# Performance work log

Hardware: AMD Instinct MI355X
Metric: run time of the kernel (lower is better)

Reference implementation:

```python
import jax, jax.numpy as jnp
import numpy as np

# Hardcoded hyperparameters from the torch module
E = 128   # n_embd
H = 4     # n_head
HS = 32   # head_size = n_embd // n_head
L = 4     # n_layer
T = 512   # block_size (full context)
V = 512   # vocab_size (quantization_levels)
B = 64    # batch
SCALE = 0.02  # init std per _init_weights


def _ln(x, g, b):
    mu = x.mean(-1, keepdims=True)
    var = ((x - mu) ** 2).mean(-1, keepdims=True)
    return (x - mu) / jnp.sqrt(var + 1e-5) * g + b


def setup_inputs() -> dict:
    key = jax.random.key(0)
    ks = jax.random.split(key, 24)
    rn = lambda k, shape: SCALE * jax.random.normal(k, shape, dtype=jnp.float32)
    return {
        "idx": jax.random.randint(ks[0], (B, T), 0, V),
        "tok_emb": rn(ks[1], (V, E)),
        "pos_emb": rn(ks[2], (T, E)),
        # per-head projections, stacked over layers and heads: x[...,E] @ wq[l,h] -> [...,HS]
        "wq": rn(ks[3], (L, H, E, HS)),
        "wk": rn(ks[4], (L, H, E, HS)),
        "wv": rn(ks[5], (L, H, E, HS)),
        "w_proj": rn(ks[6], (L, E, E)),   # torch Linear weight layout [out, in]
        "b_proj": jnp.zeros((L, E), jnp.float32),
        "ln1_g": jnp.ones((L, E), jnp.float32),
        "ln1_b": jnp.zeros((L, E), jnp.float32),
        "ln2_g": jnp.ones((L, E), jnp.float32),
        "ln2_b": jnp.zeros((L, E), jnp.float32),
        "w1": rn(ks[7], (L, 4 * E, E)),
        "b1": jnp.zeros((L, 4 * E), jnp.float32),
        "w2": rn(ks[8], (L, E, 4 * E)),
        "b2": jnp.zeros((L, E), jnp.float32),
        "lnf_g": jnp.ones((E,), jnp.float32),
        "lnf_b": jnp.zeros((E,), jnp.float32),
        "w_head": rn(ks[9], (V, E)),
        "b_head": jnp.zeros((V,), jnp.float32),
    }


def reference(idx, tok_emb, pos_emb, wq, wk, wv, w_proj, b_proj,
              ln1_g, ln1_b, ln2_g, ln2_b, w1, b1, w2, b2,
              lnf_g, lnf_b, w_head, b_head):
    Bv, Tv = idx.shape
    x = tok_emb[idx] + pos_emb[None, :Tv, :]          # [B,T,E]
    causal = jnp.tril(jnp.ones((Tv, Tv), dtype=bool))
    for l in range(L):
        h = _ln(x, ln1_g[l], ln1_b[l])
        q = jnp.einsum('bte,hed->bhtd', h, wq[l])     # [B,H,T,HS]
        k = jnp.einsum('bte,hed->bhtd', h, wk[l])
        v = jnp.einsum('bte,hed->bhtd', h, wv[l])
        s = jnp.einsum('bhtd,bhsd->bhts', q, k) * (HS ** -0.5)
        s = jnp.where(causal, s, -jnp.inf)
        a = jax.nn.softmax(s, axis=-1)
        o = jnp.einsum('bhts,bhsd->bhtd', a, v)       # [B,H,T,HS]
        o = o.transpose(0, 2, 1, 3).reshape(Bv, Tv, E)  # concat heads
        x = x + o @ w_proj[l].T + b_proj[l]
        h = _ln(x, ln2_g[l], ln2_b[l])
        x = x + jax.nn.gelu(h @ w1[l].T + b1[l], approximate=False) @ w2[l].T + b2[l]
    x = _ln(x, lnf_g, lnf_b)
    logits = x @ w_head.T + b_head                    # [B,T,V]
    return logits
```

## Files before the change

### kernel.cpp

```cpp
#include <hip/hip_runtime.h>

typedef __bf16 bf16x8 __attribute__((ext_vector_type(8)));
typedef __bf16 bf16x2 __attribute__((ext_vector_type(2)));
typedef float f32x4 __attribute__((ext_vector_type(4)));

constexpr int E_ = 128, H_ = 4, HS_ = 32, L_ = 4, T_ = 512, V_ = 512, B_ = 64;
constexpr int M_ = B_ * T_;

__device__ __forceinline__ float b2f(ushort u) {
    return __uint_as_float(((uint)u) << 16);
}
__device__ __forceinline__ ushort f2b(float f) {
    uint x = __float_as_uint(f);
    uint r = (x + 0x7fffu + ((x >> 16) & 1u)) >> 16;
    return (ushort)r;
}
__device__ __forceinline__ uint packbf(float a, float b) {
    bf16x2 t; t[0] = (__bf16)a; t[1] = (__bf16)b;
    return __builtin_bit_cast(uint, t);
}

constexpr int kNSeg = 19;
constexpr int kOffs[kNSeg + 1] = {
    0, 65536, 131072, 196608, 262144, 327680, 393216, 393728, 394240, 394752,
    395264, 395776, 657920, 659968, 922112, 922624, 922752, 922880, 988416, 988928
};
constexpr int kTotal = 988928;

struct SrcPtrs { const void* p[kNSeg]; };

__global__ __launch_bounds__(256) void k_convert(SrcPtrs sp, ushort* __restrict__ arena) {
    int gid = blockIdx.x * 256 + threadIdx.x;
    if (gid >= kTotal) return;
    bool isf32 = (((const uint*)sp.p[7])[0] == 0x3F800000u);
    int s = 0;
    #pragma unroll
    for (int i = 1; i < kNSeg; i++) if (gid >= kOffs[i]) s = i;
    int local = gid - kOffs[s];
    ushort v;
    if (isf32) v = f2b(((const float*)sp.p[s])[local]);
    else       v = ((const ushort*)sp.p[s])[local];
    arena[gid] = v;
}

__global__ void k_prep_qkv(const ushort* __restrict__ wq, const ushort* __restrict__ wk,
                           const ushort* __restrict__ wv, ushort* __restrict__ wt) {
    int gid = blockIdx.x * 256 + threadIdx.x;
    if (gid >= L_ * 384 * E_) return;
    int e = gid & 127;
    int n = (gid >> 7) % 384;
    int l = gid / (384 * E_);
    int part = n >> 7, within = n & 127, hh = within >> 5, d = within & 31;
    const ushort* src = part == 0 ? wq : (part == 1 ? wk : wv);
    wt[gid] = src[(((size_t)(l * H_ + hh) * E_) + e) * HS_ + d];
}

__global__ __launch_bounds__(256) void k_embed_ln(const int* __restrict__ idx,
                                                  const ushort* __restrict__ tok,
                                                  const ushort* __restrict__ pos,
                                                  const ushort* __restrict__ g,
                                                  const ushort* __restrict__ beta,
                                                  float* __restrict__ x, ushort* __restrict__ h) {
    int wave = threadIdx.x >> 6, lane = threadIdx.x & 63;
    int row = blockIdx.x * 4 + wave;
    int t = row & (T_ - 1);
    int id = idx[row];
    float v0 = b2f(tok[id * E_ + lane])      + b2f(pos[t * E_ + lane]);
    float v1 = b2f(tok[id * E_ + lane + 64]) + b2f(pos[t * E_ + lane + 64]);
    size_t o = (size_t)row * E_;
    x[o + lane] = v0; x[o + lane + 64] = v1;
    float s = v0 + v1;
    #pragma unroll
    for (int m = 32; m; m >>= 1) s += __shfl_xor(s, m, 64);
    float mu = s * (1.0f / 128.0f);
    float d0 = v0 - mu, d1 = v1 - mu;
    float ss = d0 * d0 + d1 * d1;
    #pragma unroll
    for (int m = 32; m; m >>= 1) ss += __shfl_xor(ss, m, 64);
    float rstd = rsqrtf(ss * (1.0f / 128.0f) + 1e-5f);
    h[o + lane]      = f2b(d0 * rstd * b2f(g[lane])      + b2f(beta[lane]));
    h[o + lane + 64] = f2b(d1 * rstd * b2f(g[lane + 64]) + b2f(beta[lane + 64]));
}

template<int EPI>
__global__ __launch_bounds__(256) void k_gemm(const ushort* __restrict__ A, const ushort* __restrict__ W,
                                              const ushort* __restrict__ bias, void* __restrict__ outp,
                                              void* __restrict__ outp2,
                                              const ushort* __restrict__ lng, const ushort* __restrict__ lnb,
                                              const uint* __restrict__ dtraw, int K, int lda, int ldc) {
    int wid = threadIdx.x >> 6, lane = threadIdx.x & 63;
    int wr = wid >> 1, wc = wid & 1;
    int bm = blockIdx.x, bn = blockIdx.y;
    int r16 = lane & 15, kq = lane >> 4;
    const ushort* Abase = A + (size_t)(bm * 128 + wr * 64 + r16) * lda + kq * 8;
    const ushort* Wbase = W + (size_t)(bn * 128 + wc * 64 + r16) * K + kq * 8;
    bool f32out = false;
    if constexpr (EPI == 1) f32out = (dtraw[0] == 0x3F800000u);
    f32x4 acc[4][4];
    #pragma unroll
    for (int i = 0; i < 4; i++)
        #pragma unroll
        for (int j = 0; j < 4; j++) acc[i][j] = (f32x4)0.0f;
    for (int k0 = 0; k0 < K; k0 += 32) {
        bf16x8 af[4], wf[4];
        #pragma unroll
        for (int mi = 0; mi < 4; mi++)
            af[mi] = *(const bf16x8*)(Abase + (size_t)mi * 16 * lda + k0);
        #pragma unroll
        for (int ni = 0; ni < 4; ni++)
            wf[ni] = *(const bf16x8*)(Wbase + (size_t)ni * 16 * K + k0);
        #pragma unroll
        for (int mi = 0; mi < 4; mi++)
            #pragma unroll
            for (int ni = 0; ni < 4; ni++)
                acc[mi][ni] = __builtin_amdgcn_mfma_f32_16x16x32_bf16(af[mi], wf[ni], acc[mi][ni], 0, 0, 0);
    }
    int orow0 = bm * 128 + wr * 64 + kq * 4;
    int ocol0 = bn * 128 + wc * 64 + r16;
    if constexpr (EPI == 5) {
        __shared__ float lnS[2][128], lnQ[2][128];
        float*  xg = (float*)outp;
        ushort* hg = (ushort*)outp2;
        #pragma unroll
        for (int ni = 0; ni < 4; ni++) {
            int col = ocol0 + ni * 16;
            float bv = b2f(bias[col]);
            #pragma unroll
            for (int mi = 0; mi < 4; mi++) {
                #pragma unroll
                for (int e = 0; e < 4; e++) {
                    size_t gi = (size_t)(orow0 + mi * 16 + e) * 128 + col;
                    float xv = xg[gi] + acc[mi][ni][e] + bv;
                    xg[gi] = xv;
                    acc[mi][ni][e] = xv;
                }
            }
        }
        #pragma unroll
        for (int mi = 0; mi < 4; mi++) {
            #pragma unroll
            for (int e = 0; e < 4; e++) {
                float s = 0.f, q = 0.f;
                #pragma unroll
                for (int ni = 0; ni < 4; ni++) { float v = acc[mi][ni][e]; s += v; q += v * v; }
                #pragma unroll
                for (int mk = 1; mk < 16; mk <<= 1) {
                    s += __shfl_xor(s, mk, 64); q += __shfl_xor(q, mk, 64);
                }
                if (r16 == 0) {
                    int lrow = wr * 64 + mi * 16 + kq * 4 + e;
                    lnS[wc][lrow] = s; lnQ[wc][lrow] = q;
                }
            }
        }
        __syncthreads();
        float gc[4], bc[4];
        #pragma unroll
        for (int ni = 0; ni < 4; ni++) {
            int col = ocol0 + ni * 16;
            gc[ni] = b2f(lng[col]); bc[ni] = b2f(lnb[col]);
        }
        #pragma unroll
        for (int mi = 0; mi < 4; mi++) {
            #pragma unroll
            for (int e = 0; e < 4; e++) {
                int lrow = wr * 64 + mi * 16 + kq * 4 + e;
                float tot = lnS[0][lrow] + lnS[1][lrow];
                float tq  = lnQ[0][lrow] + lnQ[1][lrow];
                float mu  = tot * (1.0f / 128.0f);
                float var = tq * (1.0f / 128.0f) - mu * mu;
                float rstd = rsqrtf(var + 1e-5f);
                size_t grow = (size_t)(bm * 128 + lrow) * 128;
                #pragma unroll
                for (int ni = 0; ni < 4; ni++) {
                    int col = ocol0 + ni * 16;
                    hg[grow + col] = f2b((acc[mi][ni][e] - mu) * rstd * gc[ni] + bc[ni]);
                }
            }
        }
        return;
    }
    if constexpr (EPI == 4) {
        if (bn == 2) {
            ushort* vt = (ushort*)outp2;
            #pragma unroll
            for (int mi = 0; mi < 4; mi++) {
                int row0 = orow0 + mi * 16;
                int bb = row0 >> 9, tt = row0 & 511;
                #pragma unroll
                for (int ni = 0; ni < 4; ni++) {
                    int vd = (ocol0 - 256) + ni * 16;
                    int hh = vd >> 5, dd = vd & 31;
                    ushort4 pk;
                    pk.x = f2b(acc[mi][ni][0]); pk.y = f2b(acc[mi][ni][1]);
                    pk.z = f2b(acc[mi][ni][2]); pk.w = f2b(acc[mi][ni][3]);
                    *(ushort4*)(vt + (((size_t)(bb * 4 + hh) * 32 + dd) << 9) + tt) = pk;
                }
            }
            return;
        }
    }
    #pragma unroll
    for (int mi = 0; mi < 4; mi++) {
        #pragma unroll
        for (int ni = 0; ni < 4; ni++) {
            int col = ocol0 + ni * 16;
            float bv = 0.0f;
            if constexpr (EPI == 1 || EPI == 2) bv = b2f(bias[col]);
            #pragma unroll
            for (int e = 0; e < 4; e++) {
                int row = orow0 + mi * 16 + e;
                float v = acc[mi][ni][e] + bv;
                if constexpr (EPI == 2) v = 0.5f * v * (1.0f + erff(v * 0.70710678118f));
                if constexpr (EPI == 1) {
                    if (f32out) ((float*)outp)[(size_t)row * ldc + col] = v;
                    else        ((ushort*)outp)[(size_t)row * ldc + col] = f2b(v);
                } else {
                    ((ushort*)outp)[(size_t)row * ldc + col] = f2b(v);
                }
            }
        }
    }
}

constexpr float SC_ = 0.2550348637f;

__device__ __forceinline__ bf16x8 scale8(bf16x8 v, float s) {
    bf16x8 r;
    #pragma unroll
    for (int i = 0; i < 8; i++) r[i] = (__bf16)((float)v[i] * s);
    return r;
}

__device__ __forceinline__ bf16x8 relayoutP(const float* p, int r16, int g) {
    uint pk00 = packbf(p[0], p[1]), pk01 = packbf(p[2], p[3]);
    uint pk10 = packbf(p[4], p[5]), pk11 = packbf(p[6], p[7]);
    int ga = ((g & 1) << 5) + r16;
    int gb = ga + 16;
    uint A0 = (uint)__shfl((int)pk00, ga), A1 = (uint)__shfl((int)pk01, ga);
    uint C0 = (uint)__shfl((int)pk00, gb), C1 = (uint)__shfl((int)pk01, gb);
    uint B0 = (uint)__shfl((int)pk10, ga), B1 = (uint)__shfl((int)pk11, ga);
    uint D0 = (uint)__shfl((int)pk10, gb), D1 = (uint)__shfl((int)pk11, gb);
    bool hi2 = g >= 2;
    uint4 pr;
    pr.x = hi2 ? B0 : A0; pr.y = hi2 ? B1 : A1;
    pr.z = hi2 ? D0 : C0; pr.w = hi2 ? D1 : C1;
    return __builtin_bit_cast(bf16x8, pr);
}

__global__ __launch_bounds__(256) void k_attn_mfma(const ushort* __restrict__ qk,
                                                   const ushort* __restrict__ vt,
                                                   ushort* __restrict__ o) {
    int lane = threadIdx.x & 63, w = threadIdx.x >> 6;
    int id = blockIdx.x;
    int xcd = id & 7, grp = id >> 3;
    int bh = (xcd << 5) | (grp >> 2);
    int qs = grp & 3;
    int b = bh >> 2, h = bh & 3;
    int r16 = lane & 15, g = lane >> 4;
    int iA = qs * 4 + w;
    int qbaseA = iA * 16, qbaseB = (31 - iA) * 16;
    int myqA = qbaseA + r16, myqB = qbaseB + r16;
    int qmaxA = qbaseA + 15, qmaxB = qbaseB + 15;
    const ushort* qkbase = qk + (size_t)b * 512 * 256;
    bf16x8 qfA = scale8(*(const bf16x8*)(qkbase + (size_t)(qbaseA + r16) * 256 + h * 32 + g * 8), SC_);
    bf16x8 qfB = scale8(*(const bf16x8*)(qkbase + (size_t)(qbaseB + r16) * 256 + h * 32 + g * 8), SC_);
    const ushort* kptr = qkbase + 128 + h * 32 + g * 8;
    const ushort* vbase = vt + ((size_t)bh * 32) * 512;

    f32x4 oA0 = (f32x4)0.0f, oA1 = (f32x4)0.0f, oB0 = (f32x4)0.0f, oB1 = (f32x4)0.0f;
    float psA = 0.0f, psB = 0.0f;
    for (int j0 = 0; j0 <= qmaxB; j0 += 32) {
        bf16x8 kf0 = *(const bf16x8*)(kptr + (size_t)(j0 + r16) * 256);
        bf16x8 kf1 = *(const bf16x8*)(kptr + (size_t)(j0 + 16 + r16) * 256);
        bf16x8 vf0 = *(const bf16x8*)(vbase + (size_t)r16 * 512 + j0 + g * 8);
        bf16x8 vf1 = *(const bf16x8*)(vbase + (size_t)(16 + r16) * 512 + j0 + g * 8);
        {
            f32x4 s0 = __builtin_amdgcn_mfma_f32_16x16x32_bf16(kf0, qfB, (f32x4)0.0f, 0, 0, 0);
            f32x4 s1 = __builtin_amdgcn_mfma_f32_16x16x32_bf16(kf1, qfB, (f32x4)0.0f, 0, 0, 0);
            float p[8];
            #pragma unroll
            for (int e = 0; e < 4; e++) {
                int ja = j0 + 4 * g + e;
                p[e]     = (ja      <= myqB) ? exp2f(s0[e]) : 0.0f;
                p[4 + e] = (ja + 16 <= myqB) ? exp2f(s1[e]) : 0.0f;
                psB += p[e] + p[4 + e];
            }
            bf16x8 pf = relayoutP(p, r16, g);
            oB0 = __builtin_amdgcn_mfma_f32_16x16x32_bf16(vf0, pf, oB0, 0, 0, 0);
            oB1 = __builtin_amdgcn_mfma_f32_16x16x32_bf16(vf1, pf, oB1, 0, 0, 0);
        }
        if (j0 <= qmaxA) {
            f32x4 s0 = __builtin_amdgcn_mfma_f32_16x16x32_bf16(kf0, qfA, (f32x4)0.0f, 0, 0, 0);
            f32x4 s1 = __builtin_amdgcn_mfma_f32_16x16x32_bf16(kf1, qfA, (f32x4)0.0f, 0, 0, 0);
            float p[8];
            #pragma unroll
            for (int e = 0; e < 4; e++) {
                int ja = j0 + 4 * g + e;
                p[e]     = (ja      <= myqA) ? exp2f(s0[e]) : 0.0f;
                p[4 + e] = (ja + 16 <= myqA) ? exp2f(s1[e]) : 0.0f;
                psA += p[e] + p[4 + e];
            }
            bf16x8 pf = relayoutP(p, r16, g);
            oA0 = __builtin_amdgcn_mfma_f32_16x16x32_bf16(vf0, pf, oA0, 0, 0, 0);
            oA1 = __builtin_amdgcn_mfma_f32_16x16x32_bf16(vf1, pf, oA1, 0, 0, 0);
        }
    }
    psA += __shfl_xor(psA, 16, 64); psA += __shfl_xor(psA, 32, 64);
    psB += __shfl_xor(psB, 16, 64); psB += __shfl_xor(psB, 32, 64);
    {
        float inv = 1.0f / psA;
        ushort4 w0, w1;
        w0.x = f2b(oA0[0] * inv); w0.y = f2b(oA0[1] * inv);
        w0.z = f2b(oA0[2] * inv); w0.w = f2b(oA0[3] * inv);
        w1.x = f2b(oA1[0] * inv); w1.y = f2b(oA1[1] * inv);
        w1.z = f2b(oA1[2] * inv); w1.w = f2b(oA1[3] * inv);
        size_t orow = (size_t)(b * 512 + qbaseA + r16) * 128 + h * 32;
        *(ushort4*)(o + orow + g * 4)      = w0;
        *(ushort4*)(o + orow + 16 + g * 4) = w1;
    }
    {
        float inv = 1.0f / psB;
        ushort4 w0, w1;
        w0.x = f2b(oB0[0] * inv); w0.y = f2b(oB0[1] * inv);
        w0.z = f2b(oB0[2] * inv); w0.w = f2b(oB0[3] * inv);
        w1.x = f2b(oB1[0] * inv); w1.y = f2b(oB1[1] * inv);
        w1.z = f2b(oB1[2] * inv); w1.w = f2b(oB1[3] * inv);
        size_t orow = (size_t)(b * 512 + qbaseB + r16) * 128 + h * 32;
        *(ushort4*)(o + orow + g * 4)      = w0;
        *(ushort4*)(o + orow + 16 + g * 4) = w1;
    }
}

extern "C" void kernel_launch(void* const* d_in, const int* in_sizes, int n_in,
                              void* d_out, int out_size, void* d_ws, size_t ws_size,
                              hipStream_t stream) {
    const int* idx = (const int*)d_in[0];

    char* ws = (char*)d_ws;
    float*  x     = (float*) (ws + 0);
    ushort* h     = (ushort*)(ws + (16u << 20));
    ushort* wqkvt = (ushort*)(ws + (24u << 20));
    ushort* arena = (ushort*)(ws + (25u << 20));

    ushort* qkv = (ushort*)d_out;
    ushort* o   = (ushort*)d_out + (8u << 20);
    ushort* vt  = (ushort*)d_out + (12u << 20);
    ushort* mid = (ushort*)d_out;

    const ushort* tok    = arena + kOffs[0];
    const ushort* pos    = arena + kOffs[1];
    const ushort* wqp    = arena + kOffs[2];
    const ushort* wkp    = arena + kOffs[3];
    const ushort* wvp    = arena + kOffs[4];
    const ushort* w_proj = arena + kOffs[5];
    const ushort* b_proj = arena + kOffs[6];
    const ushort* ln1_g  = arena + kOffs[7];
    const ushort* ln1_b  = arena + kOffs[8];
    const ushort* ln2_g  = arena + kOffs[9];
    const ushort* ln2_b  = arena + kOffs[10];
    const ushort* w1     = arena + kOffs[11];
    const ushort* b1     = arena + kOffs[12];
    const ushort* w2     = arena + kOffs[13];
    const ushort* b2     = arena + kOffs[14];
    const ushort* lnf_g  = arena + kOffs[15];
    const ushort* lnf_b  = arena + kOffs[16];
    const ushort* w_head = arena + kOffs[17];
    const ushort* b_head = arena + kOffs[18];

    SrcPtrs sp;
    for (int i = 0; i < kNSeg; i++) sp.p[i] = d_in[i + 1];
    k_convert<<<(kTotal + 255) / 256, 256, 0, stream>>>(sp, arena);

    k_prep_qkv<<<768, 256, 0, stream>>>(wqp, wkp, wvp, wqkvt);
    k_embed_ln<<<M_ / 4, 256, 0, stream>>>(idx, tok, pos, ln1_g, ln1_b, x, h);
    for (int l = 0; l < L_; l++) {
        const ushort* ng = (l < 3) ? (ln1_g + (l + 1) * E_) : lnf_g;
        const ushort* nb = (l < 3) ? (ln1_b + (l + 1) * E_) : lnf_b;
        k_gemm<4><<<dim3(M_ / 128, 3), 256, 0, stream>>>(h, wqkvt + (size_t)l * 384 * E_, nullptr,
                                                         qkv, vt, nullptr, nullptr, nullptr, 128, 128, 256);
        k_attn_mfma<<<1024, 256, 0, stream>>>(qkv, vt, o);
        k_gemm<5><<<dim3(M_ / 128, 1), 256, 0, stream>>>(o, w_proj + (size_t)l * E_ * E_, b_proj + l * E_,
                                                         x, h, ln2_g + l * E_, ln2_b + l * E_, nullptr, 128, 128, 128);
        k_gemm<2><<<dim3(M_ / 128, 4), 256, 0, stream>>>(h, w1 + (size_t)l * 4 * E_ * E_, b1 + l * 4 * E_,
                                                         mid, nullptr, nullptr, nullptr, nullptr, 128, 128, 512);
        k_gemm<5><<<dim3(M_ / 128, 1), 256, 0, stream>>>(mid, w2 + (size_t)l * E_ * 4 * E_, b2 + l * E_,
                                                         x, h, ng, nb, nullptr, 512, 512, 128);
    }
    k_gemm<1><<<dim3(M_ / 128, 4), 256, 0, stream>>>(h, w_head, b_head, d_out, nullptr,
                                                     nullptr, nullptr, (const uint*)d_in[8], 128, 128, 512);
}
```

Before: 520.1 us.

## Fuse attention with output projection, residual add and LayerNorm

Merges the attention kernel with the following projection GEMM, bias, residual update and LN2. Each block now handles one 16-query tile for all four heads (one wave per head), stages the attention output in swizzled LDS, and applies w_proj with MFMA before the residual add and LayerNorm. This drops one launch and the round trip of the attention output through global memory. In exchange it loses the old pairing of short and long query tiles, so per-block work is causally imbalanced. Each block also does a small projection GEMM and reloads w_proj.

```diff
diff --git a/kernel.cpp b/kernel.cpp
--- a/kernel.cpp
+++ b/kernel.cpp
@@ -248,87 +248,108 @@
     return __builtin_bit_cast(bf16x8, pr);
 }
 
-__global__ __launch_bounds__(256) void k_attn_mfma(const ushort* __restrict__ qk,
+__global__ __launch_bounds__(256) void k_attn_proj(const ushort* __restrict__ qk,
                                                    const ushort* __restrict__ vt,
-                                                   ushort* __restrict__ o) {
+                                                   const ushort* __restrict__ wproj,
+                                                   const ushort* __restrict__ bproj,
+                                                   const ushort* __restrict__ lng,
+                                                   const ushort* __restrict__ lnb,
+                                                   float* __restrict__ x,
+                                                   ushort* __restrict__ h) {
+    __shared__ ushort olds[16 * 128];
+    __shared__ float lnS[4][16], lnQ[4][16];
     int lane = threadIdx.x & 63, w = threadIdx.x >> 6;
-    int id = blockIdx.x;
-    int xcd = id & 7, grp = id >> 3;
-    int bh = (xcd << 5) | (grp >> 2);
-    int qs = grp & 3;
-    int b = bh >> 2, h = bh & 3;
     int r16 = lane & 15, g = lane >> 4;
-    int iA = qs * 4 + w;
-    int qbaseA = iA * 16, qbaseB = (31 - iA) * 16;
-    int myqA = qbaseA + r16, myqB = qbaseB + r16;
-    int qmaxA = qbaseA + 15, qmaxB = qbaseB + 15;
+    int bid = blockIdx.x;
+    int b = (bid & 7) * 8 + ((bid >> 3) >> 5);
+    int i = (bid >> 3) & 31;
+    int qbase = i * 16, qmax = qbase + 15, myq = qbase + r16;
     const ushort* qkbase = qk + (size_t)b * 512 * 256;
-    bf16x8 qfA = scale8(*(const bf16x8*)(qkbase + (size_t)(qbaseA + r16) * 256 + h * 32 + g * 8), SC_);
-    bf16x8 qfB = scale8(*(const bf16x8*)(qkbase + (size_t)(qbaseB + r16) * 256 + h * 32 + g * 8), SC_);
-    const ushort* kptr = qkbase + 128 + h * 32 + g * 8;
-    const ushort* vbase = vt + ((size_t)bh * 32) * 512;
-
-    f32x4 oA0 = (f32x4)0.0f, oA1 = (f32x4)0.0f, oB0 = (f32x4)0.0f, oB1 = (f32x4)0.0f;
-    float psA = 0.0f, psB = 0.0f;
-    for (int j0 = 0; j0 <= qmaxB; j0 += 32) {
+    bf16x8 qf = scale8(*(const bf16x8*)(qkbase + (size_t)(qbase + r16) * 256 + w * 32 + g * 8), SC_);
+    const ushort* kptr = qkbase + 128 + w * 32 + g * 8;
+    const ushort* vbase = vt + ((size_t)(b * 4 + w) * 32) * 512;
+
+    f32x4 o0 = (f32x4)0.0f, o1 = (f32x4)0.0f;
+    float ps = 0.0f;
+    for (int j0 = 0; j0 <= qmax; j0 += 32) {
         bf16x8 kf0 = *(const bf16x8*)(kptr + (size_t)(j0 + r16) * 256);
         bf16x8 kf1 = *(const bf16x8*)(kptr + (size_t)(j0 + 16 + r16) * 256);
         bf16x8 vf0 = *(const bf16x8*)(vbase + (size_t)r16 * 512 + j0 + g * 8);
         bf16x8 vf1 = *(const bf16x8*)(vbase + (size_t)(16 + r16) * 512 + j0 + g * 8);
-        {
-            f32x4 s0 = __builtin_amdgcn_mfma_f32_16x16x32_bf16(kf0, qfB, (f32x4)0.0f, 0, 0, 0);
-            f32x4 s1 = __builtin_amdgcn_mfma_f32_16x16x32_bf16(kf1, qfB, (f32x4)0.0f, 0, 0, 0);
-            float p[8];
-            #pragma unroll
-            for (int e = 0; e < 4; e++) {
-                int ja = j0 + 4 * g + e;
-                p[e]     = (ja      <= myqB) ? exp2f(s0[e]) : 0.0f;
-                p[4 + e] = (ja + 16 <= myqB) ? exp2f(s1[e]) : 0.0f;
-                psB += p[e] + p[4 + e];
-            }
-            bf16x8 pf = relayoutP(p, r16, g);
-            oB0 = __builtin_amdgcn_mfma_f32_16x16x32_bf16(vf0, pf, oB0, 0, 0, 0);
-            oB1 = __builtin_amdgcn_mfma_f32_16x16x32_bf16(vf1, pf, oB1, 0, 0, 0);
-        }
-        if (j0 <= qmaxA) {
-            f32x4 s0 = __builtin_amdgcn_mfma_f32_16x16x32_bf16(kf0, qfA, (f32x4)0.0f, 0, 0, 0);
-            f32x4 s1 = __builtin_amdgcn_mfma_f32_16x16x32_bf16(kf1, qfA, (f32x4)0.0f, 0, 0, 0);
-            float p[8];
-            #pragma unroll
-            for (int e = 0; e < 4; e++) {
-                int ja = j0 + 4 * g + e;
-                p[e]     = (ja      <= myqA) ? exp2f(s0[e]) : 0.0f;
-                p[4 + e] = (ja + 16 <= myqA) ? exp2f(s1[e]) : 0.0f;
-                psA += p[e] + p[4 + e];
-            }
-            bf16x8 pf = relayoutP(p, r16, g);
-            oA0 = __builtin_amdgcn_mfma_f32_16x16x32_bf16(vf0, pf, oA0, 0, 0, 0);
-            oA1 = __builtin_amdgcn_mfma_f32_16x16x32_bf16(vf1, pf, oA1, 0, 0, 0);
-        }
-    }
-    psA += __shfl_xor(psA, 16, 64); psA += __shfl_xor(psA, 32, 64);
-    psB += __shfl_xor(psB, 16, 64); psB += __shfl_xor(psB, 32, 64);
+        f32x4 s0 = __builtin_amdgcn_mfma_f32_16x16x32_bf16(kf0, qf, (f32x4)0.0f, 0, 0, 0);
+        f32x4 s1 = __builtin_amdgcn_mfma_f32_16x16x32_bf16(kf1, qf, (f32x4)0.0f, 0, 0, 0);
+        float p[8];
+        #pragma unroll
+        for (int e = 0; e < 4; e++) {
+            int ja = j0 + 4 * g + e;
+            p[e]     = (ja      <= myq) ? exp2f(s0[e]) : 0.0f;
+            p[4 + e] = (ja + 16 <= myq) ? exp2f(s1[e]) : 0.0f;
+            ps += p[e] + p[4 + e];
+        }
+        bf16x8 pf = relayoutP(p, r16, g);
+        o0 = __builtin_amdgcn_mfma_f32_16x16x32_bf16(vf0, pf, o0, 0, 0, 0);
+        o1 = __builtin_amdgcn_mfma_f32_16x16x32_bf16(vf1, pf, o1, 0, 0, 0);
+    }
+    ps += __shfl_xor(ps, 16, 64);
+    ps += __shfl_xor(ps, 32, 64);
+    float inv = 1.0f / ps;
     {
-        float inv = 1.0f / psA;
-        ushort4 w0, w1;
-        w0.x = f2b(oA0[0] * inv); w0.y = f2b(oA0[1] * inv);
-        w0.z = f2b(oA0[2] * inv); w0.w = f2b(oA0[3] * inv);
-        w1.x = f2b(oA1[0] * inv); w1.y = f2b(oA1[1] * inv);
-        w1.z = f2b(oA1[2] * inv); w1.w = f2b(oA1[3] * inv);
-        size_t orow = (size_t)(b * 512 + qbaseA + r16) * 128 + h * 32;
-        *(ushort4*)(o + orow + g * 4)      = w0;
-        *(ushort4*)(o + orow + 16 + g * 4) = w1;
-    }
-    {
-        float inv = 1.0f / psB;
-        ushort4 w0, w1;
-        w0.x = f2b(oB0[0] * inv); w0.y = f2b(oB0[1] * inv);
-        w0.z = f2b(oB0[2] * inv); w0.w = f2b(oB0[3] * inv);
-        w1.x = f2b(oB1[0] * inv); w1.y = f2b(oB1[1] * inv);
-        w1.z = f2b(oB1[2] * inv); w1.w = f2b(oB1[3] * inv);
-        size_t orow = (size_t)(b * 512 + qbaseB + r16) * 128 + h * 32;
-        *(ushort4*)(o + orow + g * 4)      = w0;
-        *(ushort4*)(o + orow + 16 + g * 4) = w1;
+        int base = r16 * 256 + w * 64 + g * 8;
+        int sw = (r16 & 7) << 4;
+        uint2 pk0, pk1;
+        pk0.x = packbf(o0[0] * inv, o0[1] * inv); pk0.y = packbf(o0[2] * inv, o0[3] * inv);
+        pk1.x = packbf(o1[0] * inv, o1[1] * inv); pk1.y = packbf(o1[2] * inv, o1[3] * inv);
+        *(uint2*)((char*)olds + (base ^ sw))        = pk0;
+        *(uint2*)((char*)olds + ((base + 32) ^ sw)) = pk1;
+    }
+    __syncthreads();
+    f32x4 a0 = (f32x4)0.0f, a1 = (f32x4)0.0f;
+    const ushort* wp0 = wproj + (size_t)(w * 32 + r16) * 128 + g * 8;
+    const ushort* wp1 = wp0 + (size_t)16 * 128;
+    #pragma unroll
+    for (int kk = 0; kk < 4; kk++) {
+        int abyte = (r16 * 256 + kk * 64 + g * 16) ^ ((r16 & 7) << 4);
+        bf16x8 af = *(const bf16x8*)((const char*)olds + abyte);
+        bf16x8 w0 = *(const bf16x8*)(wp0 + kk * 32);
+        bf16x8 w1 = *(const bf16x8*)(wp1 + kk * 32);
+        a0 = __builtin_amdgcn_mfma_f32_16x16x32_bf16(af, w0, a0, 0, 0, 0);
+        a1 = __builtin_amdgcn_mfma_f32_16x16x32_bf16(af, w1, a1, 0, 0, 0);
+    }
+    int col0 = w * 32 + r16, col1 = col0 + 16;
+    float bv0 = b2f(bproj[col0]), bv1 = b2f(bproj[col1]);
+    float xv0[4], xv1[4];
+    #pragma unroll
+    for (int e = 0; e < 4; e++) {
+        size_t gi = (size_t)(b * 512 + qbase + g * 4 + e) * 128;
+        float v0 = x[gi + col0] + a0[e] + bv0;
+        float v1 = x[gi + col1] + a1[e] + bv1;
+        x[gi + col0] = v0; x[gi + col1] = v1;
+        xv0[e] = v0; xv1[e] = v1;
+    }
+    #pragma unroll
+    for (int e = 0; e < 4; e++) {
+        float s = xv0[e] + xv1[e];
+        float q = xv0[e] * xv0[e] + xv1[e] * xv1[e];
+        #pragma unroll
+        for (int mk = 1; mk < 16; mk <<= 1) {
+            s += __shfl_xor(s, mk, 64); q += __shfl_xor(q, mk, 64);
+        }
+        if (r16 == 0) { lnS[w][g * 4 + e] = s; lnQ[w][g * 4 + e] = q; }
+    }
+    __syncthreads();
+    float g0 = b2f(lng[col0]), g1 = b2f(lng[col1]);
+    float be0 = b2f(lnb[col0]), be1 = b2f(lnb[col1]);
+    #pragma unroll
+    for (int e = 0; e < 4; e++) {
+        int q = g * 4 + e;
+        float tot = lnS[0][q] + lnS[1][q] + lnS[2][q] + lnS[3][q];
+        float tq  = lnQ[0][q] + lnQ[1][q] + lnQ[2][q] + lnQ[3][q];
+        float mu  = tot * (1.0f / 128.0f);
+        float var = tq * (1.0f / 128.0f) - mu * mu;
+        float rstd = rsqrtf(var + 1e-5f);
+        size_t gr = (size_t)(b * 512 + qbase + q) * 128;
+        h[gr + col0] = f2b((xv0[e] - mu) * rstd * g0 + be0);
+        h[gr + col1] = f2b((xv1[e] - mu) * rstd * g1 + be1);
     }
 }
 
@@ -344,7 +365,6 @@
     ushort* arena = (ushort*)(ws + (25u << 20));
 
     ushort* qkv = (ushort*)d_out;
-    ushort* o   = (ushort*)d_out + (8u << 20);
     ushort* vt  = (ushort*)d_out + (12u << 20);
     ushort* mid = (ushort*)d_out;
 
@@ -379,9 +399,8 @@
         const ushort* nb = (l < 3) ? (ln1_b + (l + 1) * E_) : lnf_b;
         k_gemm<4><<<dim3(M_ / 128, 3), 256, 0, stream>>>(h, wqkvt + (size_t)l * 384 * E_, nullptr,
                                                          qkv, vt, nullptr, nullptr, nullptr, 128, 128, 256);
-        k_attn_mfma<<<1024, 256, 0, stream>>>(qkv, vt, o);
-        k_gemm<5><<<dim3(M_ / 128, 1), 256, 0, stream>>>(o, w_proj + (size_t)l * E_ * E_, b_proj + l * E_,
-                                                         x, h, ln2_g + l * E_, ln2_b + l * E_, nullptr, 128, 128, 128);
+        k_attn_proj<<<2048, 256, 0, stream>>>(qkv, vt, w_proj + (size_t)l * E_ * E_, b_proj + l * E_,
+                                              ln2_g + l * E_, ln2_b + l * E_, x, h);
         k_gemm<2><<<dim3(M_ / 128, 4), 256, 0, stream>>>(h, w1 + (size_t)l * 4 * E_ * E_, b1 + l * 4 * E_,
                                                          mid, nullptr, nullptr, nullptr, nullptr, 128, 128, 512);
         k_gemm<5><<<dim3(M_ / 128, 1), 256, 0, stream>>>(mid, w2 + (size_t)l * E_ * 4 * E_, b2 + l * E_,
```

Measured after the change: 550.7 us. 5.9% more time.
